# Kernel optimization log

Measured on AMD Instinct MI355X. Metric: run time of the kernel, lower is better.

## Reference

```python
import jax, jax.numpy as jnp
import numpy as np
from jax import lax

M_SLOTS = 8192      # memory rows
N_DIM = 4096        # memory width; == FVS*FVS
FVS = 64            # function_vector_size
PLEN = 64           # max_program_length (== FVS so program->key fc is consistent)
CDIM = 256          # controller_dim
NIN, NOUT = 512, 512
STEPS = 8           # program length (number of program_i steps)
EPS = 1e-8


def setup_inputs() -> dict:
    key = jax.random.key(0)
    ks = jax.random.split(key, 15)
    s = 0.05
    stdev = 1.0 / np.sqrt(N_DIM + M_SLOTS)  # matches initalize_state uniform init
    return {
        "x": jax.random.normal(ks[0], (1, NIN), jnp.float32),
        "program": jax.random.normal(ks[1], (1, STEPS, PLEN), jnp.float32),
        "memory0": jax.random.uniform(ks[2], (M_SLOTS, N_DIM), jnp.float32, -stdev, stdev),
        "input_embedding": jax.random.normal(ks[3], (NIN, FVS), jnp.float32) * s,
        "output_embedding": jax.random.normal(ks[4], (FVS, NOUT), jnp.float32) * s,
        "Wc": jax.random.normal(ks[5], (CDIM, FVS + PLEN), jnp.float32) * s,
        "bc": jnp.zeros((CDIM,), jnp.float32),
        "Wk": jax.random.normal(ks[6], (N_DIM, CDIM), jnp.float32) * s,
        "bk": jnp.zeros((N_DIM,), jnp.float32),
        "We": jax.random.normal(ks[7], (N_DIM, CDIM), jnp.float32) * s,
        "be": jnp.zeros((N_DIM,), jnp.float32),
        "Wa": jax.random.normal(ks[8], (N_DIM, CDIM), jnp.float32) * s,
        "ba": jnp.zeros((N_DIM,), jnp.float32),
        "Wrk": jax.random.normal(ks[9], (N_DIM, PLEN), jnp.float32) * s,
        "brk": jnp.zeros((N_DIM,), jnp.float32),
    }


def _cosine_address(mem, k):
    # mem: [M, N], k: [N] -> softmax over M of cosine similarity (content addressing)
    sim = mem @ k  # [M]
    denom = jnp.sqrt(jnp.sum(mem * mem, axis=1)) * jnp.sqrt(jnp.sum(k * k)) + EPS
    return jax.nn.softmax(sim / denom)  # [M]


def _ntm_forward(x, program, memory0, input_embedding, output_embedding,
                 Wc, bc, Wk, bk, We, be, Wa, ba, Wrk, brk):
    X = x @ input_embedding  # [1, FVS]

    def step(carry, prog_t):
        Xc, mem = carry  # Xc: [1, FVS], mem: [M, N]
        # Controller: sigmoid(Linear(concat(X, program_i)))
        c = jax.nn.sigmoid(jnp.concatenate([Xc[0], prog_t]) @ Wc.T + bc)  # [CDIM]
        # Write head: key / erase / add from controller state, content addressing
        k = jnp.tanh(c @ Wk.T + bk)           # [N]
        e = jax.nn.sigmoid(c @ We.T + be)     # [N]
        a = jnp.tanh(c @ Wa.T + ba)           # [N]
        ww = _cosine_address(mem, k)          # [M]
        mem = mem * (1.0 - ww[:, None] * e[None, :]) + ww[:, None] * a[None, :]
        # Read head: key from program vector, content addressing on updated memory
        kr = jnp.tanh(prog_t @ Wrk.T + brk)   # [N]
        wr = _cosine_address(mem, kr)         # [M]
        read = wr @ mem                       # [N] == last_read
        # Executioner: X <- tanh(X @ last_read.view(FVS, FVS))
        Xn = jnp.tanh(Xc @ read.reshape(FVS, FVS))  # [1, FVS]
        return (Xn, mem), None

    (Xf, _memf), _ = lax.scan(step, (X, memory0), program[0])
    return Xf @ output_embedding  # [1, NOUT]


def reference(x, program, memory0, input_embedding, output_embedding,
              Wc, bc, Wk, bk, We, be, Wa, ba, Wrk, brk):
    return _ntm_forward(x, program, memory0, input_embedding, output_embedding,
                        Wc, bc, Wk, bk, We, be, Wa, ba, Wrk, brk)
```

## Files before the change

kernel.cpp:

```cpp
#include <hip/hip_runtime.h>
#include <math.h>

#define M_SLOTS 8192
#define N_DIM   4096
#define FVS     64
#define PLEN    64
#define CDIM    256
#define NIN     512
#define NOUT    512
#define STEPS   8
#define EPS_F   1e-8f

#define SROWS   32
#define NSB     (M_SLOTS / SROWS)
#define RROWS   32
#define NRB     (M_SLOTS / RROWS)


__device__ inline float wave_sum(float v) {
    for (int off = 32; off; off >>= 1) v += __shfl_down(v, off);
    return v;
}

__device__ inline float blk_sum_1024(float v, float* sh) {
    v = wave_sum(v);
    int lane = threadIdx.x & 63, wid = threadIdx.x >> 6;
    if (lane == 0) sh[wid] = v;
    __syncthreads();
    if (threadIdx.x < 16) {
        v = sh[threadIdx.x];
        for (int off = 8; off; off >>= 1) v += __shfl_down(v, off);
        if (threadIdx.x == 0) sh[16] = v;
    }
    __syncthreads();
    float r = sh[16];
    __syncthreads();
    return r;
}

__device__ inline void group_reduce8(float v[8], int lane) {
    float t0, t1, t2, t3;
    t0 = __shfl_xor((lane & 1) ? v[0] : v[4], 1);
    t1 = __shfl_xor((lane & 1) ? v[1] : v[5], 1);
    t2 = __shfl_xor((lane & 1) ? v[2] : v[6], 1);
    t3 = __shfl_xor((lane & 1) ? v[3] : v[7], 1);
    v[0] = ((lane & 1) ? v[4] : v[0]) + t0;
    v[1] = ((lane & 1) ? v[5] : v[1]) + t1;
    v[2] = ((lane & 1) ? v[6] : v[2]) + t2;
    v[3] = ((lane & 1) ? v[7] : v[3]) + t3;
    t0 = __shfl_xor((lane & 2) ? v[0] : v[2], 2);
    t1 = __shfl_xor((lane & 2) ? v[1] : v[3], 2);
    v[0] = ((lane & 2) ? v[2] : v[0]) + t0;
    v[1] = ((lane & 2) ? v[3] : v[1]) + t1;
    t0 = __shfl_xor((lane & 4) ? v[0] : v[1], 4);
    v[0] = ((lane & 4) ? v[1] : v[0]) + t0;
}


__global__ void k_init_ctrl(const float* __restrict__ x, const float* __restrict__ emb,
                            const float* __restrict__ prog0,
                            const float* __restrict__ Wc, const float* __restrict__ bc,
                            float* __restrict__ X, float* __restrict__ c) {
    __shared__ float in[FVS + PLEN];
    int tid = threadIdx.x;
    if (tid < FVS) {
        float acc = 0.f;
        for (int i = 0; i < NIN; ++i) acc += x[i] * emb[i * FVS + tid];
        X[tid] = acc;
        in[tid] = acc;
    } else if (tid < FVS + PLEN) {
        in[tid] = prog0[tid - FVS];
    }
    __syncthreads();
    float acc = bc[tid];
    const float* wrow = Wc + tid * (FVS + PLEN);
    #pragma unroll 8
    for (int i = 0; i < FVS + PLEN; ++i) acc += wrow[i] * in[i];
    c[tid] = 1.f / (1.f + expf(-acc));
}

__device__ inline void keys_row(int gw, float4 cv, int lane, const float* __restrict__ prog,
                                const float* __restrict__ Wk, const float* __restrict__ bk,
                                const float* __restrict__ We, const float* __restrict__ be,
                                const float* __restrict__ Wa, const float* __restrict__ ba,
                                const float* __restrict__ Wrk, const float* __restrict__ brk,
                                float* __restrict__ k, float* __restrict__ e,
                                float* __restrict__ a, float* __restrict__ kr,
                                float* __restrict__ ekr, float* __restrict__ ea,
                                float* __restrict__ e2) {
    float4 wv;
    wv = ((const float4*)(Wk + (size_t)gw * CDIM))[lane];
    float sK = wv.x*cv.x + wv.y*cv.y + wv.z*cv.z + wv.w*cv.w;
    wv = ((const float4*)(We + (size_t)gw * CDIM))[lane];
    float sE = wv.x*cv.x + wv.y*cv.y + wv.z*cv.z + wv.w*cv.w;
    wv = ((const float4*)(Wa + (size_t)gw * CDIM))[lane];
    float sA = wv.x*cv.x + wv.y*cv.y + wv.z*cv.z + wv.w*cv.w;
    float sR = Wrk[(size_t)gw * PLEN + lane] * prog[lane];
    sK = wave_sum(sK); sE = wave_sum(sE); sA = wave_sum(sA); sR = wave_sum(sR);
    if (lane == 0) {
        float ev  = 1.f / (1.f + expf(-(sE + be[gw])));
        float av  = tanhf(sA + ba[gw]);
        float krv = tanhf(sR + brk[gw]);
        k[gw]   = tanhf(sK + bk[gw]);
        e[gw]   = ev;
        a[gw]   = av;
        kr[gw]  = krv;
        ekr[gw] = ev * krv;
        ea[gw]  = ev * av;
        e2[gw]  = ev * ev;
    }
}

__global__ __launch_bounds__(256) void k_keys4(
        const float* __restrict__ c, const float* __restrict__ prog,
        const float* __restrict__ Wk, const float* __restrict__ bk,
        const float* __restrict__ We, const float* __restrict__ be,
        const float* __restrict__ Wa, const float* __restrict__ ba,
        const float* __restrict__ Wrk, const float* __restrict__ brk,
        float* __restrict__ k, float* __restrict__ e,
        float* __restrict__ a, float* __restrict__ kr,
        float* __restrict__ ekr, float* __restrict__ ea, float* __restrict__ e2) {
    int lane = threadIdx.x & 63, wid = threadIdx.x >> 6;
    const float4 cv = ((const float4*)c)[lane];
    for (int gw = blockIdx.x * 4 + wid; gw < 4096; gw += 2048)
        keys_row(gw, cv, lane, prog, Wk, bk, We, be, Wa, ba, Wrk, brk,
                 k, e, a, kr, ekr, ea, e2);
}


template<int NUP>
__global__ __launch_bounds__(256) void k_stats(
        const float* __restrict__ mem0,
        const float* __restrict__ ehist, const float* __restrict__ ahist,
        const float* __restrict__ wwhist,
        const float* __restrict__ kc, const float* __restrict__ krc,
        const float* __restrict__ ekrc, const float* __restrict__ eac,
        const float* __restrict__ e2c,
        float* __restrict__ stat4) {
    const int tid  = threadIdx.x;
    const int cc   = blockIdx.x;
    const int rb   = blockIdx.y;
    const int col4 = cc * 256 + tid;
    const int lane = tid & 63, wid = tid >> 6;
    const int HN   = (NUP > 0) ? NUP : 1;
    float4 eh[HN], ah[HN];
    #pragma unroll
    for (int s = 0; s < NUP; ++s) {
        eh[s] = ((const float4*)(ehist + (size_t)s * N_DIM))[col4];
        ah[s] = ((const float4*)(ahist + (size_t)s * N_DIM))[col4];
    }
    const float4 kk  = ((const float4*)kc)[col4];
    const float4 rr  = ((const float4*)krc)[col4];
    const float4 fkr = ((const float4*)ekrc)[col4];
    const float4 fea = ((const float4*)eac)[col4];
    const float4 fe2 = ((const float4*)e2c)[col4];
    const float4 ce  = ((const float4*)(ehist + (size_t)NUP * N_DIM))[col4];
    const float4 ca  = ((const float4*)(ahist + (size_t)NUP * N_DIM))[col4];

    __shared__ float shc[4][SROWS][64];

    #pragma unroll
    for (int r = 0; r < SROWS; ++r) {
        const int m = rb * SROWS + r;
        float4 v = ((const float4*)(mem0 + (size_t)m * N_DIM))[col4];
        #pragma unroll
        for (int s = 0; s < NUP; ++s) {
            float w = wwhist[(size_t)s * M_SLOTS + m];
            v.x = v.x * (1.f - w * eh[s].x) + w * ah[s].x;
            v.y = v.y * (1.f - w * eh[s].y) + w * ah[s].y;
            v.z = v.z * (1.f - w * eh[s].z) + w * ah[s].z;
            v.w = v.w * (1.f - w * eh[s].w) + w * ah[s].w;
        }
        float sv[8] = {0.f, 0.f, 0.f, 0.f, 0.f, 0.f, 0.f, 0.f};
        #define ACC1(vv,kc_,rc_,ekr_,ac_,ea_,ec_,e2_) { \
            float _v = vv; float _v2 = _v * _v; \
            sv[0] += _v * kc_;  sv[1] += _v * rc_;  sv[2] += _v * ekr_; \
            sv[3] += _v * ac_;  sv[4] += _v * ea_;  sv[5] += _v * _v; \
            sv[6] += _v2 * ec_; sv[7] += _v2 * e2_; }
        ACC1(v.x, kk.x, rr.x, fkr.x, ca.x, fea.x, ce.x, fe2.x)
        ACC1(v.y, kk.y, rr.y, fkr.y, ca.y, fea.y, ce.y, fe2.y)
        ACC1(v.z, kk.z, rr.z, fkr.z, ca.z, fea.z, ce.z, fe2.z)
        ACC1(v.w, kk.w, rr.w, fkr.w, ca.w, fea.w, ce.w, fe2.w)
        #undef ACC1
        group_reduce8(sv, lane);
        {
            const int st = ((lane & 1) << 2) | (lane & 2) | ((lane & 4) >> 2);
            shc[wid][r][(lane & 56) + st] = sv[0];
        }
    }
    __syncthreads();
    {
        const int r = tid >> 3, st = tid & 7;
        float tot = 0.f;
        #pragma unroll
        for (int w = 0; w < 4; ++w)
            #pragma unroll
            for (int g = 0; g < 8; ++g)
                tot += shc[w][r][g * 8 + st];
        stat4[(size_t)(cc * 8 + st) * M_SLOTS + rb * SROWS + r] = tot;
    }
}

template<int NUP>
__global__ __launch_bounds__(256) void k_read(
        const float* __restrict__ mem0,
        const float* __restrict__ ehist, const float* __restrict__ ahist,
        const float* __restrict__ wwhist,
        const float* __restrict__ wr,
        float* __restrict__ partial) {
    const int tid  = threadIdx.x;
    const int cc   = blockIdx.x;
    const int rb   = blockIdx.y;
    const int col4 = cc * 256 + tid;
    float4 eh[NUP], ah[NUP];
    #pragma unroll
    for (int s = 0; s < NUP; ++s) {
        eh[s] = ((const float4*)(ehist + (size_t)s * N_DIM))[col4];
        ah[s] = ((const float4*)(ahist + (size_t)s * N_DIM))[col4];
    }
    float4 acc = make_float4(0.f, 0.f, 0.f, 0.f);
    for (int r = 0; r < RROWS; ++r) {
        const int m = rb * RROWS + r;
        float4 v = ((const float4*)(mem0 + (size_t)m * N_DIM))[col4];
        #pragma unroll
        for (int s = 0; s < NUP; ++s) {
            float w = wwhist[(size_t)s * M_SLOTS + m];
            v.x = v.x * (1.f - w * eh[s].x) + w * ah[s].x;
            v.y = v.y * (1.f - w * eh[s].y) + w * ah[s].y;
            v.z = v.z * (1.f - w * eh[s].z) + w * ah[s].z;
            v.w = v.w * (1.f - w * eh[s].w) + w * ah[s].w;
        }
        float w2 = wr[m];
        acc.x += w2 * v.x; acc.y += w2 * v.y; acc.z += w2 * v.z; acc.w += w2 * v.w;
    }
    ((float4*)partial)[(size_t)rb * (N_DIM / 4) + col4] = acc;
}

__global__ __launch_bounds__(1024) void k_addr(
        const float* __restrict__ kc, const float* __restrict__ krc,
        const float* __restrict__ ac,
        const float* __restrict__ stat4,
        float* __restrict__ ww, float* __restrict__ wr) {
    __shared__ float sh[17];
    int tid = threadIdx.x;
    float a0=0, a1=0, a2=0, a3=0;
    for (int i = tid; i < N_DIM; i += 1024) {
        float kv = kc[i], rv = krc[i], av = ac[i];
        a0 += kv*kv; a1 += rv*rv; a2 += av*rv; a3 += av*av;
    }
    float d0 = blk_sum_1024(a0, sh);
    float d1 = blk_sum_1024(a1, sh);
    float d2 = blk_sum_1024(a2, sh);
    float d3 = blk_sum_1024(a3, sh);
    float knorm = sqrtf(d0), krnorm = sqrtf(d1);

    #define ST(st, m) (stat4[(size_t)(st) * M_SLOTS + (m)] \
                     + stat4[(size_t)((st) + 8) * M_SLOTS + (m)] \
                     + stat4[(size_t)((st) + 16) * M_SLOTS + (m)] \
                     + stat4[(size_t)((st) + 24) * M_SLOTS + (m)])
    float ex[M_SLOTS / 1024];
    float n2l[M_SLOTS / 1024];
    float ls = 0.f;
    #pragma unroll
    for (int j = 0; j < M_SLOTS / 1024; ++j) {
        int m = tid + j * 1024;
        float n2 = ST(5, m);
        n2l[j] = n2;
        float v = ST(0, m) / (sqrtf(n2) * knorm + EPS_F);
        ex[j] = expf(v);
        ls += ex[j];
    }
    ls = blk_sum_1024(ls, sh);
    float inv = 1.f / ls;
    float wv[M_SLOTS / 1024];
    #pragma unroll
    for (int j = 0; j < M_SLOTS / 1024; ++j) {
        wv[j] = ex[j] * inv;
        ww[tid + j * 1024] = wv[j];
    }
    float ls2 = 0.f;
    #pragma unroll
    for (int j = 0; j < M_SLOTS / 1024; ++j) {
        int m = tid + j * 1024;
        float w1 = wv[j];
        float sim2 = ST(1, m) - w1 * ST(2, m) + w1 * d2;
        float n2n  = n2l[j] - 2.f*w1*ST(6, m) + w1*w1*ST(7, m)
                   + 2.f*w1*ST(3, m) - 2.f*w1*w1*ST(4, m) + w1*w1*d3;
        float v = sim2 / (sqrtf(n2n) * krnorm + EPS_F);
        ex[j] = expf(v);
        ls2 += ex[j];
    }
    #undef ST
    ls2 = blk_sum_1024(ls2, sh);
    float inv2 = 1.f / ls2;
    #pragma unroll
    for (int j = 0; j < M_SLOTS / 1024; ++j) wr[tid + j * 1024] = ex[j] * inv2;
}

__global__ void k_read_reduce(const float* __restrict__ partial, float* __restrict__ red) {
    __shared__ float gsh[4][64];
    int l = threadIdx.x & 63;
    int q = threadIdx.x >> 6;
    int c = blockIdx.x * 64 + l;
    float acc = 0.f;
    #pragma unroll 8
    for (int r = q * (NRB / 4); r < (q + 1) * (NRB / 4); ++r)
        acc += partial[(size_t)r * N_DIM + c];
    gsh[q][l] = acc;
    __syncthreads();
    if (threadIdx.x < 64)
        red[blockIdx.x * 64 + threadIdx.x] =
            gsh[0][threadIdx.x] + gsh[1][threadIdx.x] + gsh[2][threadIdx.x] + gsh[3][threadIdx.x];
}

__global__ __launch_bounds__(256) void k_exec_keys(
        const float* __restrict__ Xold, float* __restrict__ Xnew,
        const float* __restrict__ red, const float* __restrict__ prog_next,
        const float* __restrict__ Wc, const float* __restrict__ bc,
        const float* __restrict__ Wk, const float* __restrict__ bk,
        const float* __restrict__ We, const float* __restrict__ be,
        const float* __restrict__ Wa, const float* __restrict__ ba,
        const float* __restrict__ Wrk, const float* __restrict__ brk,
        float* __restrict__ k, float* __restrict__ e,
        float* __restrict__ a, float* __restrict__ kr,
        float* __restrict__ ekr, float* __restrict__ ea, float* __restrict__ e2) {
    __shared__ float xo[FVS];
    __shared__ float xs[FVS];
    __shared__ float cc[CDIM];
    int tid = threadIdx.x, lane = tid & 63, wid = tid >> 6;
    if (tid < FVS) xo[tid] = Xold[tid];
    __syncthreads();
    if (tid < FVS) {
        float acc = 0.f;
        #pragma unroll
        for (int i = 0; i < FVS; ++i) acc += xo[i] * red[i * FVS + tid];
        float xn = tanhf(acc);
        xs[tid] = xn;
        if (blockIdx.x == 0) Xnew[tid] = xn;
    }
    __syncthreads();
    {
        float acc = bc[tid];
        const float* wrow = Wc + tid * (FVS + PLEN);
        #pragma unroll
        for (int i = 0; i < FVS; ++i) acc += wrow[i] * xs[i];
        #pragma unroll
        for (int i = 0; i < PLEN; ++i) acc += wrow[FVS + i] * prog_next[i];
        cc[tid] = 1.f / (1.f + expf(-acc));
    }
    __syncthreads();
    const float4 cv = ((const float4*)cc)[lane];
    for (int gw = blockIdx.x * 4 + wid; gw < 4096; gw += 2048)
        keys_row(gw, cv, lane, prog_next, Wk, bk, We, be, Wa, ba, Wrk, brk,
                 k, e, a, kr, ekr, ea, e2);
}

__global__ void k_final(const float* __restrict__ Xold, const float* __restrict__ red,
                        const float* __restrict__ out_emb, float* __restrict__ out) {
    __shared__ float xo[FVS];
    __shared__ float xs[FVS];
    int tid = threadIdx.x;
    if (tid < FVS) xo[tid] = Xold[tid];
    __syncthreads();
    if (tid < FVS) {
        float acc = 0.f;
        #pragma unroll
        for (int i = 0; i < FVS; ++i) acc += xo[i] * red[i * FVS + tid];
        xs[tid] = tanhf(acc);
    }
    __syncthreads();
    for (int col = tid; col < NOUT; col += 256) {
        float acc = 0.f;
        #pragma unroll
        for (int i = 0; i < FVS; ++i) acc += xs[i] * out_emb[i * NOUT + col];
        out[col] = acc;
    }
}


typedef void (*stats_fn)(const float*, const float*, const float*, const float*,
                         const float*, const float*, const float*, const float*,
                         const float*, float*);
typedef void (*read_fn)(const float*, const float*, const float*, const float*,
                        const float*, float*);

extern "C" void kernel_launch(void* const* d_in, const int* in_sizes, int n_in,
                              void* d_out, int out_size, void* d_ws, size_t ws_size,
                              hipStream_t stream) {
    const float* x        = (const float*)d_in[0];
    const float* program  = (const float*)d_in[1];
    const float* memory0  = (const float*)d_in[2];
    const float* in_emb   = (const float*)d_in[3];
    const float* out_emb  = (const float*)d_in[4];
    const float* Wc       = (const float*)d_in[5];
    const float* bc       = (const float*)d_in[6];
    const float* Wk       = (const float*)d_in[7];
    const float* bk       = (const float*)d_in[8];
    const float* We       = (const float*)d_in[9];
    const float* be       = (const float*)d_in[10];
    const float* Wa       = (const float*)d_in[11];
    const float* ba       = (const float*)d_in[12];
    const float* Wrk      = (const float*)d_in[13];
    const float* brk      = (const float*)d_in[14];
    float* out = (float*)d_out;

    float* ws = (float*)d_ws;
    size_t off = 0;
    float* ehist   = ws + off; off += (size_t)STEPS * N_DIM;
    float* ahist   = ws + off; off += (size_t)STEPS * N_DIM;
    float* wwhist  = ws + off; off += (size_t)STEPS * M_SLOTS;
    float* kcur    = ws + off; off += N_DIM;
    float* krcur   = ws + off; off += N_DIM;
    float* ekrcur  = ws + off; off += N_DIM;
    float* eacur   = ws + off; off += N_DIM;
    float* e2cur   = ws + off; off += N_DIM;
    float* stat4   = ws + off; off += (size_t)32 * M_SLOTS;
    float* partial = ws + off; off += (size_t)NRB * N_DIM;
    float* wrcur   = ws + off; off += M_SLOTS;
    float* red     = ws + off; off += N_DIM;
    float* Xb0     = ws + off; off += FVS;
    float* Xb1     = ws + off; off += FVS;
    float* c       = ws + off; off += CDIM;

    static const stats_fn SF[STEPS] = {
        k_stats<0>, k_stats<1>, k_stats<2>, k_stats<3>,
        k_stats<4>, k_stats<5>, k_stats<6>, k_stats<7> };
    static const read_fn RF[STEPS] = {
        k_read<1>, k_read<2>, k_read<3>, k_read<4>,
        k_read<5>, k_read<6>, k_read<7>, k_read<8> };

    k_init_ctrl<<<1, 256, 0, stream>>>(x, in_emb, program, Wc, bc, Xb0, c);
    k_keys4<<<512, 256, 0, stream>>>(c, program, Wk, bk, We, be, Wa, ba, Wrk, brk,
                                     kcur, ehist, ahist, krcur, ekrcur, eacur, e2cur);

    for (int t = 0; t < STEPS; ++t) {
        SF[t]<<<dim3(4, NSB), 256, 0, stream>>>(
            memory0, ehist, ahist, wwhist, kcur, krcur, ekrcur, eacur, e2cur, stat4);
        k_addr<<<1, 1024, 0, stream>>>(kcur, krcur, ahist + (size_t)t * N_DIM,
                                       stat4, wwhist + (size_t)t * M_SLOTS, wrcur);
        RF[t]<<<dim3(4, NRB), 256, 0, stream>>>(
            memory0, ehist, ahist, wwhist, wrcur, partial);
        k_read_reduce<<<64, 256, 0, stream>>>(partial, red);

        const float* Xcur = (t & 1) ? Xb1 : Xb0;
        float*       Xnxt = (t & 1) ? Xb0 : Xb1;
        if (t < STEPS - 1) {
            k_exec_keys<<<512, 256, 0, stream>>>(
                Xcur, Xnxt, red, program + (t + 1) * PLEN,
                Wc, bc, Wk, bk, We, be, Wa, ba, Wrk, brk,
                kcur, ehist + (size_t)(t + 1) * N_DIM,
                ahist + (size_t)(t + 1) * N_DIM, krcur, ekrcur, eacur, e2cur);
        } else {
            k_final<<<1, 256, 0, stream>>>(Xcur, red, out_emb, out);
        }
    }
}
```

Baseline: 778.0 us.

## Checkpoint memory after four steps to cap update replay depth

The read kernel at step 3 now writes the fully updated memory into a workspace buffer. Steps 4-7 then replay only up to four updates from that checkpoint instead of up to eight from memory0, which cuts the per-row FMA work in the stats and read kernels. The stats kernel also caches the write weights in shared memory, prefetches eight rows into registers, and halves its row block size. In exchange there is one extra 128 MB write pass and a larger workspace.

```diff
diff --git a/kernel.cpp b/kernel.cpp
--- a/kernel.cpp
+++ b/kernel.cpp
@@ -11,7 +11,7 @@
 #define STEPS   8
 #define EPS_F   1e-8f
 
-#define SROWS   32
+#define SROWS   16
 #define NSB     (M_SLOTS / SROWS)
 #define RROWS   32
 #define NRB     (M_SLOTS / RROWS)
@@ -130,7 +130,7 @@
 
 template<int NUP>
 __global__ __launch_bounds__(256) void k_stats(
-        const float* __restrict__ mem0,
+        const float* __restrict__ base,
         const float* __restrict__ ehist, const float* __restrict__ ahist,
         const float* __restrict__ wwhist,
         const float* __restrict__ kc, const float* __restrict__ krc,
@@ -143,6 +143,15 @@
     const int col4 = cc * 256 + tid;
     const int lane = tid & 63, wid = tid >> 6;
     const int HN   = (NUP > 0) ? NUP : 1;
+
+    __shared__ float wws[HN][SROWS];
+    __shared__ float shc[4][SROWS][64];
+
+    if (NUP > 0 && tid < NUP * SROWS) {
+        const int s = tid / SROWS, r = tid - s * SROWS;
+        wws[s][r] = wwhist[(size_t)s * M_SLOTS + rb * SROWS + r];
+    }
+
     float4 eh[HN], ah[HN];
     #pragma unroll
     for (int s = 0; s < NUP; ++s) {
@@ -157,15 +166,23 @@
     const float4 ce  = ((const float4*)(ehist + (size_t)NUP * N_DIM))[col4];
     const float4 ca  = ((const float4*)(ahist + (size_t)NUP * N_DIM))[col4];
 
-    __shared__ float shc[4][SROWS][64];
+    if (NUP > 0) __syncthreads();
+
+    const float4* mb = (const float4*)base;
+    const size_t rs  = N_DIM / 4;
+    const size_t bi  = (size_t)(rb * SROWS) * rs + col4;
+
+    float4 vb[8];
+    #pragma unroll
+    for (int r = 0; r < 8; ++r) vb[r] = mb[bi + (size_t)r * rs];
 
     #pragma unroll
     for (int r = 0; r < SROWS; ++r) {
-        const int m = rb * SROWS + r;
-        float4 v = ((const float4*)(mem0 + (size_t)m * N_DIM))[col4];
+        float4 v = vb[r & 7];
+        if (r + 8 < SROWS) vb[r & 7] = mb[bi + (size_t)(r + 8) * rs];
         #pragma unroll
         for (int s = 0; s < NUP; ++s) {
-            float w = wwhist[(size_t)s * M_SLOTS + m];
+            const float w = wws[s][r];
             v.x = v.x * (1.f - w * eh[s].x) + w * ah[s].x;
             v.y = v.y * (1.f - w * eh[s].y) + w * ah[s].y;
             v.z = v.z * (1.f - w * eh[s].z) + w * ah[s].z;
@@ -189,7 +206,7 @@
         }
     }
     __syncthreads();
-    {
+    if (tid < SROWS * 8) {
         const int r = tid >> 3, st = tid & 7;
         float tot = 0.f;
         #pragma unroll
@@ -201,13 +218,13 @@
     }
 }
 
-template<int NUP>
+template<int NUP, bool STORE>
 __global__ __launch_bounds__(256) void k_read(
-        const float* __restrict__ mem0,
+        const float* __restrict__ base,
         const float* __restrict__ ehist, const float* __restrict__ ahist,
         const float* __restrict__ wwhist,
         const float* __restrict__ wr,
-        float* __restrict__ partial) {
+        float* __restrict__ partial, float* __restrict__ dst) {
     const int tid  = threadIdx.x;
     const int cc   = blockIdx.x;
     const int rb   = blockIdx.y;
@@ -221,7 +238,7 @@
     float4 acc = make_float4(0.f, 0.f, 0.f, 0.f);
     for (int r = 0; r < RROWS; ++r) {
         const int m = rb * RROWS + r;
-        float4 v = ((const float4*)(mem0 + (size_t)m * N_DIM))[col4];
+        float4 v = ((const float4*)(base + (size_t)m * N_DIM))[col4];
         #pragma unroll
         for (int s = 0; s < NUP; ++s) {
             float w = wwhist[(size_t)s * M_SLOTS + m];
@@ -230,6 +247,7 @@
             v.z = v.z * (1.f - w * eh[s].z) + w * ah[s].z;
             v.w = v.w * (1.f - w * eh[s].w) + w * ah[s].w;
         }
+        if (STORE) ((float4*)dst)[(size_t)m * (N_DIM / 4) + col4] = v;
         float w2 = wr[m];
         acc.x += w2 * v.x; acc.y += w2 * v.y; acc.z += w2 * v.z; acc.w += w2 * v.w;
     }
@@ -377,12 +395,6 @@
     }
 }
 
-
-typedef void (*stats_fn)(const float*, const float*, const float*, const float*,
-                         const float*, const float*, const float*, const float*,
-                         const float*, float*);
-typedef void (*read_fn)(const float*, const float*, const float*, const float*,
-                        const float*, float*);
 
 extern "C" void kernel_launch(void* const* d_in, const int* in_sizes, int n_in,
                               void* d_out, int out_size, void* d_ws, size_t ws_size,
@@ -406,6 +418,7 @@
 
     float* ws = (float*)d_ws;
     size_t off = 0;
+    float* mem4    = ws + off; off += (size_t)M_SLOTS * N_DIM;
     float* ehist   = ws + off; off += (size_t)STEPS * N_DIM;
     float* ahist   = ws + off; off += (size_t)STEPS * N_DIM;
     float* wwhist  = ws + off; off += (size_t)STEPS * M_SLOTS;
@@ -422,24 +435,50 @@
     float* Xb1     = ws + off; off += FVS;
     float* c       = ws + off; off += CDIM;
 
-    static const stats_fn SF[STEPS] = {
-        k_stats<0>, k_stats<1>, k_stats<2>, k_stats<3>,
-        k_stats<4>, k_stats<5>, k_stats<6>, k_stats<7> };
-    static const read_fn RF[STEPS] = {
-        k_read<1>, k_read<2>, k_read<3>, k_read<4>,
-        k_read<5>, k_read<6>, k_read<7>, k_read<8> };
-
     k_init_ctrl<<<1, 256, 0, stream>>>(x, in_emb, program, Wc, bc, Xb0, c);
     k_keys4<<<512, 256, 0, stream>>>(c, program, Wk, bk, We, be, Wa, ba, Wrk, brk,
                                      kcur, ehist, ahist, krcur, ekrcur, eacur, e2cur);
 
+    const dim3 sgrid(4, NSB), rgrid(4, NRB);
+
     for (int t = 0; t < STEPS; ++t) {
-        SF[t]<<<dim3(4, NSB), 256, 0, stream>>>(
-            memory0, ehist, ahist, wwhist, kcur, krcur, ekrcur, eacur, e2cur, stat4);
+        const float* sb  = (t < 4) ? memory0 : mem4;
+        const float* ehs = (t < 4) ? ehist  : ehist  + (size_t)4 * N_DIM;
+        const float* ahs = (t < 4) ? ahist  : ahist  + (size_t)4 * N_DIM;
+        const float* wws = (t < 4) ? wwhist : wwhist + (size_t)4 * M_SLOTS;
+
+        switch (t & 3) {
+            case 0: k_stats<0><<<sgrid, 256, 0, stream>>>(sb, ehs, ahs, wws,
+                        kcur, krcur, ekrcur, eacur, e2cur, stat4); break;
+            case 1: k_stats<1><<<sgrid, 256, 0, stream>>>(sb, ehs, ahs, wws,
+                        kcur, krcur, ekrcur, eacur, e2cur, stat4); break;
+            case 2: k_stats<2><<<sgrid, 256, 0, stream>>>(sb, ehs, ahs, wws,
+                        kcur, krcur, ekrcur, eacur, e2cur, stat4); break;
+            case 3: k_stats<3><<<sgrid, 256, 0, stream>>>(sb, ehs, ahs, wws,
+                        kcur, krcur, ekrcur, eacur, e2cur, stat4); break;
+        }
+
         k_addr<<<1, 1024, 0, stream>>>(kcur, krcur, ahist + (size_t)t * N_DIM,
                                        stat4, wwhist + (size_t)t * M_SLOTS, wrcur);
-        RF[t]<<<dim3(4, NRB), 256, 0, stream>>>(
-            memory0, ehist, ahist, wwhist, wrcur, partial);
+
+        switch (t) {
+            case 0: k_read<1,false><<<rgrid, 256, 0, stream>>>(sb, ehs, ahs, wws,
+                        wrcur, partial, nullptr); break;
+            case 1: k_read<2,false><<<rgrid, 256, 0, stream>>>(sb, ehs, ahs, wws,
+                        wrcur, partial, nullptr); break;
+            case 2: k_read<3,false><<<rgrid, 256, 0, stream>>>(sb, ehs, ahs, wws,
+                        wrcur, partial, nullptr); break;
+            case 3: k_read<4,true ><<<rgrid, 256, 0, stream>>>(sb, ehs, ahs, wws,
+                        wrcur, partial, mem4); break;
+            case 4: k_read<1,false><<<rgrid, 256, 0, stream>>>(sb, ehs, ahs, wws,
+                        wrcur, partial, nullptr); break;
+            case 5: k_read<2,false><<<rgrid, 256, 0, stream>>>(sb, ehs, ahs, wws,
+                        wrcur, partial, nullptr); break;
+            case 6: k_read<3,false><<<rgrid, 256, 0, stream>>>(sb, ehs, ahs, wws,
+                        wrcur, partial, nullptr); break;
+            case 7: k_read<4,false><<<rgrid, 256, 0, stream>>>(sb, ehs, ahs, wws,
+                        wrcur, partial, nullptr); break;
+        }
         k_read_reduce<<<64, 256, 0, stream>>>(partial, red);
 
         const float* Xcur = (t & 1) ? Xb1 : Xb0;
```

After: 796.2 us. 2.3% more time.

## Split single-block addressing kernel and fuse read-softmax into the read pass

Applied to the files above, without the earlier changes.

Replaces the single 1024-thread addressing kernel with a 16-block kernel that computes the write-head exponentials and partial sums. The read-weight computation and its normalisation move into the read kernel and the reduce kernel, and the current step's write update is applied inline using shared-memory weights. The goal is to remove a serial single-block bottleneck that runs once per step. In exchange, every read block recomputes the key-norm dot products over 4096 elements and reads the 16 partial sums.

```diff
diff --git a/kernel.cpp b/kernel.cpp
--- a/kernel.cpp
+++ b/kernel.cpp
@@ -22,18 +22,12 @@
     return v;
 }
 
-__device__ inline float blk_sum_1024(float v, float* sh) {
+__device__ inline float blk_sum_256(float v, float* sh) {
     v = wave_sum(v);
     int lane = threadIdx.x & 63, wid = threadIdx.x >> 6;
     if (lane == 0) sh[wid] = v;
     __syncthreads();
-    if (threadIdx.x < 16) {
-        v = sh[threadIdx.x];
-        for (int off = 8; off; off >>= 1) v += __shfl_down(v, off);
-        if (threadIdx.x == 0) sh[16] = v;
-    }
-    __syncthreads();
-    float r = sh[16];
+    float r = sh[0] + sh[1] + sh[2] + sh[3];
     __syncthreads();
     return r;
 }
@@ -201,104 +195,140 @@
     }
 }
 
-template<int NUP>
+#define ST4(st, m) (stat4[(size_t)(st) * M_SLOTS + (m)] \
+                  + stat4[(size_t)((st) + 8) * M_SLOTS + (m)] \
+                  + stat4[(size_t)((st) + 16) * M_SLOTS + (m)] \
+                  + stat4[(size_t)((st) + 24) * M_SLOTS + (m)])
+
+__global__ __launch_bounds__(256) void k_addrA(
+        const float* __restrict__ kc, const float* __restrict__ stat4,
+        float* __restrict__ exp1, float* __restrict__ n2sav,
+        float* __restrict__ psum1) {
+    __shared__ float sh4[4];
+    const int tid = threadIdx.x, b = blockIdx.x;
+    float a0 = 0.f;
+    for (int i = tid; i < N_DIM; i += 256) { float kv = kc[i]; a0 += kv * kv; }
+    float d0 = blk_sum_256(a0, sh4);
+    float knorm = sqrtf(d0);
+    float ls = 0.f;
+    #pragma unroll
+    for (int j = 0; j < 2; ++j) {
+        int m = b * 512 + j * 256 + tid;
+        float sim = ST4(0, m);
+        float n2  = ST4(5, m);
+        float v = sim / (sqrtf(n2) * knorm + EPS_F);
+        float ex = expf(v);
+        exp1[m] = ex;
+        n2sav[m] = n2;
+        ls += ex;
+    }
+    float tot = blk_sum_256(ls, sh4);
+    if (tid == 0) psum1[b] = tot;
+}
+
+template<int NHIST>
 __global__ __launch_bounds__(256) void k_read(
         const float* __restrict__ mem0,
         const float* __restrict__ ehist, const float* __restrict__ ahist,
         const float* __restrict__ wwhist,
-        const float* __restrict__ wr,
+        const float* __restrict__ krc,
+        const float* __restrict__ exp1, const float* __restrict__ n2sav,
+        const float* __restrict__ psum1, const float* __restrict__ stat4,
+        float* __restrict__ ww, float* __restrict__ psum2,
         float* __restrict__ partial) {
     const int tid  = threadIdx.x;
     const int cc   = blockIdx.x;
     const int rb   = blockIdx.y;
     const int col4 = cc * 256 + tid;
-    float4 eh[NUP], ah[NUP];
+
+    __shared__ float sh4[4];
+    __shared__ float w1s[RROWS];
+    __shared__ float wrs[RROWS];
+
+    const float* ac = ahist + (size_t)NHIST * N_DIM;
+    float a1 = 0.f, a2 = 0.f, a3 = 0.f;
+    for (int i = tid; i < N_DIM; i += 256) {
+        float rv = krc[i], av = ac[i];
+        a1 += rv * rv; a2 += av * rv; a3 += av * av;
+    }
+    float d1 = blk_sum_256(a1, sh4);
+    float d2 = blk_sum_256(a2, sh4);
+    float d3 = blk_sum_256(a3, sh4);
+    float krnorm = sqrtf(d1);
+
+    float s1 = 0.f;
     #pragma unroll
-    for (int s = 0; s < NUP; ++s) {
+    for (int i = 0; i < 16; ++i) s1 += psum1[i];
+    const float inv1 = 1.f / s1;
+
+    if (tid < RROWS) {
+        const int m = rb * RROWS + tid;
+        float w1 = exp1[m] * inv1;
+        w1s[tid] = w1;
+        float skr  = ST4(1, m);
+        float sekr = ST4(2, m);
+        float sa_  = ST4(3, m);
+        float sea_ = ST4(4, m);
+        float qe_  = ST4(6, m);
+        float qe2_ = ST4(7, m);
+        float sim2 = skr - w1 * sekr + w1 * d2;
+        float n2n  = n2sav[m] - 2.f*w1*qe_ + w1*w1*qe2_
+                   + 2.f*w1*sa_ - 2.f*w1*w1*sea_ + w1*w1*d3;
+        float v2 = sim2 / (sqrtf(n2n) * krnorm + EPS_F);
+        wrs[tid] = expf(v2);
+        if (cc == 0) ww[m] = w1;
+    }
+    __syncthreads();
+    if (cc == 0 && tid == 0) {
+        float s = 0.f;
+        #pragma unroll
+        for (int r = 0; r < RROWS; ++r) s += wrs[r];
+        psum2[rb] = s;
+    }
+
+    const int HN = (NHIST > 0) ? NHIST : 1;
+    float4 eh[HN], ah[HN];
+    #pragma unroll
+    for (int s = 0; s < NHIST; ++s) {
         eh[s] = ((const float4*)(ehist + (size_t)s * N_DIM))[col4];
         ah[s] = ((const float4*)(ahist + (size_t)s * N_DIM))[col4];
     }
+    const float4 ce = ((const float4*)(ehist + (size_t)NHIST * N_DIM))[col4];
+    const float4 ca = ((const float4*)(ahist + (size_t)NHIST * N_DIM))[col4];
+
     float4 acc = make_float4(0.f, 0.f, 0.f, 0.f);
     for (int r = 0; r < RROWS; ++r) {
         const int m = rb * RROWS + r;
         float4 v = ((const float4*)(mem0 + (size_t)m * N_DIM))[col4];
         #pragma unroll
-        for (int s = 0; s < NUP; ++s) {
+        for (int s = 0; s < NHIST; ++s) {
             float w = wwhist[(size_t)s * M_SLOTS + m];
             v.x = v.x * (1.f - w * eh[s].x) + w * ah[s].x;
             v.y = v.y * (1.f - w * eh[s].y) + w * ah[s].y;
             v.z = v.z * (1.f - w * eh[s].z) + w * ah[s].z;
             v.w = v.w * (1.f - w * eh[s].w) + w * ah[s].w;
         }
-        float w2 = wr[m];
+        {
+            const float w1 = w1s[r];
+            v.x = v.x * (1.f - w1 * ce.x) + w1 * ca.x;
+            v.y = v.y * (1.f - w1 * ce.y) + w1 * ca.y;
+            v.z = v.z * (1.f - w1 * ce.z) + w1 * ca.z;
+            v.w = v.w * (1.f - w1 * ce.w) + w1 * ca.w;
+        }
+        const float w2 = wrs[r];
         acc.x += w2 * v.x; acc.y += w2 * v.y; acc.z += w2 * v.z; acc.w += w2 * v.w;
     }
     ((float4*)partial)[(size_t)rb * (N_DIM / 4) + col4] = acc;
 }
 
-__global__ __launch_bounds__(1024) void k_addr(
-        const float* __restrict__ kc, const float* __restrict__ krc,
-        const float* __restrict__ ac,
-        const float* __restrict__ stat4,
-        float* __restrict__ ww, float* __restrict__ wr) {
-    __shared__ float sh[17];
-    int tid = threadIdx.x;
-    float a0=0, a1=0, a2=0, a3=0;
-    for (int i = tid; i < N_DIM; i += 1024) {
-        float kv = kc[i], rv = krc[i], av = ac[i];
-        a0 += kv*kv; a1 += rv*rv; a2 += av*rv; a3 += av*av;
-    }
-    float d0 = blk_sum_1024(a0, sh);
-    float d1 = blk_sum_1024(a1, sh);
-    float d2 = blk_sum_1024(a2, sh);
-    float d3 = blk_sum_1024(a3, sh);
-    float knorm = sqrtf(d0), krnorm = sqrtf(d1);
-
-    #define ST(st, m) (stat4[(size_t)(st) * M_SLOTS + (m)] \
-                     + stat4[(size_t)((st) + 8) * M_SLOTS + (m)] \
-                     + stat4[(size_t)((st) + 16) * M_SLOTS + (m)] \
-                     + stat4[(size_t)((st) + 24) * M_SLOTS + (m)])
-    float ex[M_SLOTS / 1024];
-    float n2l[M_SLOTS / 1024];
-    float ls = 0.f;
-    #pragma unroll
-    for (int j = 0; j < M_SLOTS / 1024; ++j) {
-        int m = tid + j * 1024;
-        float n2 = ST(5, m);
-        n2l[j] = n2;
-        float v = ST(0, m) / (sqrtf(n2) * knorm + EPS_F);
-        ex[j] = expf(v);
-        ls += ex[j];
-    }
-    ls = blk_sum_1024(ls, sh);
-    float inv = 1.f / ls;
-    float wv[M_SLOTS / 1024];
-    #pragma unroll
-    for (int j = 0; j < M_SLOTS / 1024; ++j) {
-        wv[j] = ex[j] * inv;
-        ww[tid + j * 1024] = wv[j];
-    }
-    float ls2 = 0.f;
-    #pragma unroll
-    for (int j = 0; j < M_SLOTS / 1024; ++j) {
-        int m = tid + j * 1024;
-        float w1 = wv[j];
-        float sim2 = ST(1, m) - w1 * ST(2, m) + w1 * d2;
-        float n2n  = n2l[j] - 2.f*w1*ST(6, m) + w1*w1*ST(7, m)
-                   + 2.f*w1*ST(3, m) - 2.f*w1*w1*ST(4, m) + w1*w1*d3;
-        float v = sim2 / (sqrtf(n2n) * krnorm + EPS_F);
-        ex[j] = expf(v);
-        ls2 += ex[j];
-    }
-    #undef ST
-    ls2 = blk_sum_1024(ls2, sh);
-    float inv2 = 1.f / ls2;
-    #pragma unroll
-    for (int j = 0; j < M_SLOTS / 1024; ++j) wr[tid + j * 1024] = ex[j] * inv2;
-}
-
-__global__ void k_read_reduce(const float* __restrict__ partial, float* __restrict__ red) {
+__global__ void k_read_reduce(const float* __restrict__ partial,
+                              const float* __restrict__ psum2,
+                              float* __restrict__ red) {
+    __shared__ float sh4[4];
     __shared__ float gsh[4][64];
+    float p = psum2[threadIdx.x];
+    float tot = blk_sum_256(p, sh4);
+    float inv2 = 1.f / tot;
     int l = threadIdx.x & 63;
     int q = threadIdx.x >> 6;
     int c = blockIdx.x * 64 + l;
@@ -309,8 +339,9 @@
     gsh[q][l] = acc;
     __syncthreads();
     if (threadIdx.x < 64)
-        red[blockIdx.x * 64 + threadIdx.x] =
-            gsh[0][threadIdx.x] + gsh[1][threadIdx.x] + gsh[2][threadIdx.x] + gsh[3][threadIdx.x];
+        red[blockIdx.x * 64 + threadIdx.x] = inv2 *
+            (gsh[0][threadIdx.x] + gsh[1][threadIdx.x] +
+             gsh[2][threadIdx.x] + gsh[3][threadIdx.x]);
 }
 
 __global__ __launch_bounds__(256) void k_exec_keys(
@@ -377,12 +408,6 @@
     }
 }
 
-
-typedef void (*stats_fn)(const float*, const float*, const float*, const float*,
-                         const float*, const float*, const float*, const float*,
-                         const float*, float*);
-typedef void (*read_fn)(const float*, const float*, const float*, const float*,
-                        const float*, float*);
 
 extern "C" void kernel_launch(void* const* d_in, const int* in_sizes, int n_in,
                               void* d_out, int out_size, void* d_ws, size_t ws_size,
@@ -416,31 +441,65 @@
     float* e2cur   = ws + off; off += N_DIM;
     float* stat4   = ws + off; off += (size_t)32 * M_SLOTS;
     float* partial = ws + off; off += (size_t)NRB * N_DIM;
-    float* wrcur   = ws + off; off += M_SLOTS;
+    float* exp1    = ws + off; off += M_SLOTS;
+    float* n2sav   = ws + off; off += M_SLOTS;
+    float* psum1   = ws + off; off += 16;
+    float* psum2   = ws + off; off += NRB;
     float* red     = ws + off; off += N_DIM;
     float* Xb0     = ws + off; off += FVS;
     float* Xb1     = ws + off; off += FVS;
     float* c       = ws + off; off += CDIM;
 
-    static const stats_fn SF[STEPS] = {
-        k_stats<0>, k_stats<1>, k_stats<2>, k_stats<3>,
-        k_stats<4>, k_stats<5>, k_stats<6>, k_stats<7> };
-    static const read_fn RF[STEPS] = {
-        k_read<1>, k_read<2>, k_read<3>, k_read<4>,
-        k_read<5>, k_read<6>, k_read<7>, k_read<8> };
-
     k_init_ctrl<<<1, 256, 0, stream>>>(x, in_emb, program, Wc, bc, Xb0, c);
     k_keys4<<<512, 256, 0, stream>>>(c, program, Wk, bk, We, be, Wa, ba, Wrk, brk,
                                      kcur, ehist, ahist, krcur, ekrcur, eacur, e2cur);
 
+    const dim3 sgrid(4, NSB), rgrid(4, NRB);
+
     for (int t = 0; t < STEPS; ++t) {
-        SF[t]<<<dim3(4, NSB), 256, 0, stream>>>(
-            memory0, ehist, ahist, wwhist, kcur, krcur, ekrcur, eacur, e2cur, stat4);
-        k_addr<<<1, 1024, 0, stream>>>(kcur, krcur, ahist + (size_t)t * N_DIM,
-                                       stat4, wwhist + (size_t)t * M_SLOTS, wrcur);
-        RF[t]<<<dim3(4, NRB), 256, 0, stream>>>(
-            memory0, ehist, ahist, wwhist, wrcur, partial);
-        k_read_reduce<<<64, 256, 0, stream>>>(partial, red);
+        float* wwslot = wwhist + (size_t)t * M_SLOTS;
+
+        switch (t) {
+            case 0: k_stats<0><<<sgrid, 256, 0, stream>>>(memory0, ehist, ahist, wwhist,
+                        kcur, krcur, ekrcur, eacur, e2cur, stat4); break;
+            case 1: k_stats<1><<<sgrid, 256, 0, stream>>>(memory0, ehist, ahist, wwhist,
+                        kcur, krcur, ekrcur, eacur, e2cur, stat4); break;
+            case 2: k_stats<2><<<sgrid, 256, 0, stream>>>(memory0, ehist, ahist, wwhist,
+                        kcur, krcur, ekrcur, eacur, e2cur, stat4); break;
+            case 3: k_stats<3><<<sgrid, 256, 0, stream>>>(memory0, ehist, ahist, wwhist,
+                        kcur, krcur, ekrcur, eacur, e2cur, stat4); break;
+            case 4: k_stats<4><<<sgrid, 256, 0, stream>>>(memory0, ehist, ahist, wwhist,
+                        kcur, krcur, ekrcur, eacur, e2cur, stat4); break;
+            case 5: k_stats<5><<<sgrid, 256, 0, stream>>>(memory0, ehist, ahist, wwhist,
+                        kcur, krcur, ekrcur, eacur, e2cur, stat4); break;
+            case 6: k_stats<6><<<sgrid, 256, 0, stream>>>(memory0, ehist, ahist, wwhist,
+                        kcur, krcur, ekrcur, eacur, e2cur, stat4); break;
+            case 7: k_stats<7><<<sgrid, 256, 0, stream>>>(memory0, ehist, ahist, wwhist,
+                        kcur, krcur, ekrcur, eacur, e2cur, stat4); break;
+        }
+
+        k_addrA<<<16, 256, 0, stream>>>(kcur, stat4, exp1, n2sav, psum1);
+
+        switch (t) {
+            case 0: k_read<0><<<rgrid, 256, 0, stream>>>(memory0, ehist, ahist, wwhist,
+                        krcur, exp1, n2sav, psum1, stat4, wwslot, psum2, partial); break;
+            case 1: k_read<1><<<rgrid, 256, 0, stream>>>(memory0, ehist, ahist, wwhist,
+                        krcur, exp1, n2sav, psum1, stat4, wwslot, psum2, partial); break;
+            case 2: k_read<2><<<rgrid, 256, 0, stream>>>(memory0, ehist, ahist, wwhist,
+                        krcur, exp1, n2sav, psum1, stat4, wwslot, psum2, partial); break;
+            case 3: k_read<3><<<rgrid, 256, 0, stream>>>(memory0, ehist, ahist, wwhist,
+                        krcur, exp1, n2sav, psum1, stat4, wwslot, psum2, partial); break;
+            case 4: k_read<4><<<rgrid, 256, 0, stream>>>(memory0, ehist, ahist, wwhist,
+                        krcur, exp1, n2sav, psum1, stat4, wwslot, psum2, partial); break;
+            case 5: k_read<5><<<rgrid, 256, 0, stream>>>(memory0, ehist, ahist, wwhist,
+                        krcur, exp1, n2sav, psum1, stat4, wwslot, psum2, partial); break;
+            case 6: k_read<6><<<rgrid, 256, 0, stream>>>(memory0, ehist, ahist, wwhist,
+                        krcur, exp1, n2sav, psum1, stat4, wwslot, psum2, partial); break;
+            case 7: k_read<7><<<rgrid, 256, 0, stream>>>(memory0, ehist, ahist, wwhist,
+                        krcur, exp1, n2sav, psum1, stat4, wwslot, psum2, partial); break;
+        }
+
+        k_read_reduce<<<64, 256, 0, stream>>>(partial, psum2, red);
 
         const float* Xcur = (t & 1) ? Xb1 : Xb0;
         float*       Xnxt = (t & 1) ? Xb0 : Xb1;
```

After: 725.5 us. 1.07x faster.
